# Kernel tuning notes

Measured on AMD Instinct MI355X. Metric: run time of the kernel, lower is better.

The kernel has to match this reference:

```python
import jax, jax.numpy as jnp
import numpy as np

N_NODES = 100000
IN_CH, HIDDEN, OUT_CH = 128, 128, 64
N_POS, N_NEG = 600000, 600000


def _glorot(key, shape):
    lim = float(np.sqrt(6.0 / (shape[0] + shape[1])))
    return jax.random.uniform(key, shape, jnp.float32, -lim, lim)


def setup_inputs() -> dict:
    key = jax.random.key(0)
    k = jax.random.split(key, 7)
    x = jax.random.normal(k[0], (N_NODES, IN_CH), jnp.float32)
    pos_edge_index = jax.random.randint(k[1], (2, N_POS), 0, N_NODES, jnp.int64)
    neg_edge_index = jax.random.randint(k[2], (2, N_NEG), 0, N_NODES, jnp.int64)
    W1 = _glorot(k[3], (IN_CH, HIDDEN))
    b1 = jnp.zeros((HIDDEN,), jnp.float32)
    W2 = _glorot(k[4], (HIDDEN, OUT_CH))
    b2 = jnp.zeros((OUT_CH,), jnp.float32)
    return {"x": x, "pos_edge_index": pos_edge_index, "neg_edge_index": neg_edge_index,
            "W1": W1, "b1": b1, "W2": W2, "b2": b2}


def gcn_conv(x, W, b, src, dst, n_nodes):
    # PyG GCNConv: add self-loops, symmetric deg^-1/2 normalization, linear, bias
    h = x @ W                                               # [N, F_out]
    ones = jnp.ones(src.shape, h.dtype)
    deg = jax.ops.segment_sum(ones, dst, num_segments=n_nodes) + 1.0  # self-loop
    dinv = jax.lax.rsqrt(deg)                               # deg^-0.5, deg >= 1
    norm = dinv[src] * dinv[dst]                            # per-edge norm
    agg = jax.ops.segment_sum(h[src] * norm[:, None], dst, num_segments=n_nodes)
    agg = agg + h * (dinv * dinv)[:, None]                  # self-loop messages
    return agg + b


def reference(x, pos_edge_index, neg_edge_index, W1, b1, W2, b2):
    n = x.shape[0]
    src, dst = pos_edge_index[0], pos_edge_index[1]
    z = gcn_conv(x, W1, b1, src, dst, n)
    z = jax.nn.relu(z)
    z = gcn_conv(z, W2, b2, src, dst, n)
    # decode: gather endpoints of pos+neg edges, elementwise product, sum over feat
    ei = jnp.concatenate([pos_edge_index, neg_edge_index], axis=-1)  # [2, E_pos+E_neg]
    return jnp.sum(z[ei[0]] * z[ei[1]], axis=-1)
```

## Files before the change

### kernel.cpp

```cpp
#include <hip/hip_runtime.h>

#define N_NODES 100000
#define IN_CH 128
#define HIDDEN 128
#define OUT_CH 64
#define N_POS 600000
#define N_NEG 600000

typedef unsigned int uint32;
typedef unsigned short ushort16;
typedef __attribute__((ext_vector_type(8))) short bf16x8;
typedef __attribute__((ext_vector_type(4))) float f32x4;

__device__ inline float bf_lo(uint32 u) {
    union { uint32 i; float f; } v;
    v.i = u << 16;
    return v.f;
}
__device__ inline float bf_hi(uint32 u) {
    union { uint32 i; float f; } v;
    v.i = u & 0xffff0000u;
    return v.f;
}
__device__ inline ushort16 f2bf(float f) {
    union { uint32 i; float f; } v;
    v.f = f;
    uint32 r = v.i + 0x7fffu + ((v.i >> 16) & 1u);
    return (ushort16)(r >> 16);
}
__device__ inline uint32 pack2bf(float a, float b) {
    return (uint32)f2bf(a) | ((uint32)f2bf(b) << 16);
}

__global__ void hist_count(const int* __restrict__ dst, int* __restrict__ hist, int n_edges) {
    int i = blockIdx.x * blockDim.x + threadIdx.x;
    if (i < n_edges) atomicAdd(&hist[dst[i]], 1);
}

__global__ void scan_reduce(const int* __restrict__ hist, int* __restrict__ partials, int n) {
    __shared__ int sdata[256];
    int b = blockIdx.x, t = threadIdx.x;
    int base = b * 1024;
    int s = 0;
    for (int i = t; i < 1024; i += 256) {
        int idx = base + i;
        s += (idx < n) ? hist[idx] : 0;
    }
    sdata[t] = s;
    __syncthreads();
    for (int off = 128; off > 0; off >>= 1) {
        if (t < off) sdata[t] += sdata[t + off];
        __syncthreads();
    }
    if (t == 0) partials[b] = sdata[0];
}

__global__ void scan_partials(int* __restrict__ partials, int nb) {
    __shared__ int tmp[128];
    int t = threadIdx.x;
    int v = (t < nb) ? partials[t] : 0;
    tmp[t] = v;
    __syncthreads();
    for (int off = 1; off < 128; off <<= 1) {
        int a = (t >= off) ? tmp[t - off] : 0;
        __syncthreads();
        tmp[t] += a;
        __syncthreads();
    }
    if (t < nb) partials[t] = tmp[t] - v;
}

__global__ void scan_final(const int* __restrict__ hist, const int* __restrict__ partials,
                           int* __restrict__ rowstart, int* __restrict__ cursor,
                           float* __restrict__ dinv, int n) {
    __shared__ int tsum[256];
    int t = threadIdx.x, b = blockIdx.x;
    int base = b * 1024 + t * 4;
    int v[4];
    int s = 0;
#pragma unroll
    for (int j = 0; j < 4; j++) {
        int i = base + j;
        v[j] = (i < n) ? hist[i] : 0;
        s += v[j];
    }
    tsum[t] = s;
    __syncthreads();
    for (int off = 1; off < 256; off <<= 1) {
        int a = (t >= off) ? tsum[t - off] : 0;
        __syncthreads();
        tsum[t] += a;
        __syncthreads();
    }
    int offset = partials[b] + (tsum[t] - s);
#pragma unroll
    for (int j = 0; j < 4; j++) {
        int i = base + j;
        if (i < n) {
            rowstart[i] = offset;
            cursor[i] = offset;
            dinv[i] = rsqrtf((float)v[j] + 1.0f);
            offset += v[j];
        }
    }
    if (b == 0 && t == 0) rowstart[n] = N_POS;
}

__global__ void csr_fill(const int* __restrict__ src, const int* __restrict__ dst,
                         const float* __restrict__ dinv, int* __restrict__ cursor,
                         int2* __restrict__ adjw, int n_edges) {
    int e = blockIdx.x * blockDim.x + threadIdx.x;
    if (e < n_edges) {
        int s = src[e], d = dst[e];
        int p = atomicAdd(&cursor[d], 1);
        adjw[p] = int2{s, __float_as_int(dinv[s] * dinv[d])};
    }
}

__global__ void wt_convert(const float* __restrict__ W1, const float* __restrict__ W2,
                           ushort16* __restrict__ W1t, ushort16* __restrict__ W2t) {
    int i = blockIdx.x * blockDim.x + threadIdx.x;
    if (i < 128 * 128) {
        int n = i >> 7, k = i & 127;
        W1t[i] = f2bf(W1[k * 128 + n]);
    } else {
        int j = i - 128 * 128;
        if (j < 64 * 128) {
            int n = j >> 7, k = j & 127;
            W2t[j] = f2bf(W2[k * 64 + n]);
        }
    }
}

template <int M, bool XBF>
__global__ __launch_bounds__(256) void gemm_mfma(const void* __restrict__ Xv,
                                                const ushort16* __restrict__ Wt,
                                                ushort16* __restrict__ H, int n) {
    constexpr int K = 128;
    constexpr int TN = 64;
    constexpr int XS = 136;
    __shared__ short Xs[TN * XS];
    __shared__ short Ws[M * XS];
    int tid = threadIdx.x;
    int node0 = blockIdx.x * TN;

    for (int q = tid; q < M * K / 8; q += 256) {
        int row = q >> 4;
        int c = q & 15;
        uint4 v = ((const uint4*)Wt)[q];
        *(uint4*)(Ws + row * XS + c * 8) = v;
    }
    if (!XBF) {
        const float* X = (const float*)Xv;
        int row = tid >> 2, part = tid & 3;
        int gn = node0 + row;
#pragma unroll
        for (int c = 0; c < 8; ++c) {
            int k = part * 32 + c * 4;
            float4 v = (gn < n) ? *(const float4*)(X + (size_t)gn * K + k) : float4{0, 0, 0, 0};
            uint2 p = {pack2bf(v.x, v.y), pack2bf(v.z, v.w)};
            *(uint2*)(Xs + row * XS + k) = p;
        }
    } else {
        const ushort16* X = (const ushort16*)Xv;
        for (int q = tid; q < TN * K / 8; q += 256) {
            int row = q >> 4;
            int c = q & 15;
            int gn = node0 + row;
            uint4 v = (gn < n) ? ((const uint4*)(X + (size_t)gn * K))[c] : uint4{0, 0, 0, 0};
            *(uint4*)(Xs + row * XS + c * 8) = v;
        }
    }
    __syncthreads();

    constexpr int CT = M / 16;
    int w = tid >> 6;
    int lane = tid & 63;
    int l15 = lane & 15;
    int quad = lane >> 4;

    f32x4 acc[CT] = {};
    const short* xrow = Xs + (w * 16 + l15) * XS + quad * 8;
#pragma unroll
    for (int kk = 0; kk < 4; ++kk) {
        bf16x8 a = *(const bf16x8*)(xrow + kk * 32);
#pragma unroll
        for (int ct = 0; ct < CT; ++ct) {
            bf16x8 b = *(const bf16x8*)(Ws + (ct * 16 + l15) * XS + quad * 8 + kk * 32);
            acc[ct] = __builtin_amdgcn_mfma_f32_16x16x32_bf16(a, b, acc[ct], 0, 0, 0);
        }
    }

#pragma unroll
    for (int ct = 0; ct < CT; ++ct) {
#pragma unroll
        for (int r = 0; r < 4; ++r) {
            int gn = node0 + w * 16 + quad * 4 + r;
            if (gn < n) H[(size_t)gn * M + ct * 16 + l15] = f2bf(acc[ct][r]);
        }
    }
}

template <int F, bool RELU>
__global__ void agg_pull(const int* __restrict__ rowstart, const int2* __restrict__ adjw,
                         const float* __restrict__ dinv, const ushort16* __restrict__ H,
                         const float* __restrict__ bias, ushort16* __restrict__ Z, int n) {
    int g = threadIdx.x >> 4;
    int l = threadIdx.x & 15;
    int node = blockIdx.x * (blockDim.x >> 4) + g;
    if (node >= n) return;
    float dn = dinv[node];
    int rs = rowstart[node], re = rowstart[node + 1];
    if (F == 128) {
        float ac[4][8] = {};
        int p = rs;
        for (; p + 4 <= re; p += 4) {
            int2 e0 = adjw[p], e1 = adjw[p + 1], e2 = adjw[p + 2], e3 = adjw[p + 3];
            uint4 h0 = *(const uint4*)(H + (size_t)e0.x * F + l * 8);
            uint4 h1 = *(const uint4*)(H + (size_t)e1.x * F + l * 8);
            uint4 h2 = *(const uint4*)(H + (size_t)e2.x * F + l * 8);
            uint4 h3 = *(const uint4*)(H + (size_t)e3.x * F + l * 8);
            float w0 = __int_as_float(e0.y), w1 = __int_as_float(e1.y);
            float w2 = __int_as_float(e2.y), w3 = __int_as_float(e3.y);
            ac[0][0] += bf_lo(h0.x) * w0; ac[0][1] += bf_hi(h0.x) * w0;
            ac[0][2] += bf_lo(h0.y) * w0; ac[0][3] += bf_hi(h0.y) * w0;
            ac[0][4] += bf_lo(h0.z) * w0; ac[0][5] += bf_hi(h0.z) * w0;
            ac[0][6] += bf_lo(h0.w) * w0; ac[0][7] += bf_hi(h0.w) * w0;
            ac[1][0] += bf_lo(h1.x) * w1; ac[1][1] += bf_hi(h1.x) * w1;
            ac[1][2] += bf_lo(h1.y) * w1; ac[1][3] += bf_hi(h1.y) * w1;
            ac[1][4] += bf_lo(h1.z) * w1; ac[1][5] += bf_hi(h1.z) * w1;
            ac[1][6] += bf_lo(h1.w) * w1; ac[1][7] += bf_hi(h1.w) * w1;
            ac[2][0] += bf_lo(h2.x) * w2; ac[2][1] += bf_hi(h2.x) * w2;
            ac[2][2] += bf_lo(h2.y) * w2; ac[2][3] += bf_hi(h2.y) * w2;
            ac[2][4] += bf_lo(h2.z) * w2; ac[2][5] += bf_hi(h2.z) * w2;
            ac[2][6] += bf_lo(h2.w) * w2; ac[2][7] += bf_hi(h2.w) * w2;
            ac[3][0] += bf_lo(h3.x) * w3; ac[3][1] += bf_hi(h3.x) * w3;
            ac[3][2] += bf_lo(h3.y) * w3; ac[3][3] += bf_hi(h3.y) * w3;
            ac[3][4] += bf_lo(h3.z) * w3; ac[3][5] += bf_hi(h3.z) * w3;
            ac[3][6] += bf_lo(h3.w) * w3; ac[3][7] += bf_hi(h3.w) * w3;
        }
        for (; p < re; ++p) {
            int2 e = adjw[p];
            float w = __int_as_float(e.y);
            uint4 h = *(const uint4*)(H + (size_t)e.x * F + l * 8);
            ac[0][0] += bf_lo(h.x) * w; ac[0][1] += bf_hi(h.x) * w;
            ac[0][2] += bf_lo(h.y) * w; ac[0][3] += bf_hi(h.y) * w;
            ac[0][4] += bf_lo(h.z) * w; ac[0][5] += bf_hi(h.z) * w;
            ac[0][6] += bf_lo(h.w) * w; ac[0][7] += bf_hi(h.w) * w;
        }
        uint4 hv = *(const uint4*)(H + (size_t)node * F + l * 8);
        float4 bv0 = *(const float4*)(bias + l * 8);
        float4 bv1 = *(const float4*)(bias + l * 8 + 4);
        float d2 = dn * dn;
        float v[8];
        float hs[8] = {bf_lo(hv.x), bf_hi(hv.x), bf_lo(hv.y), bf_hi(hv.y),
                       bf_lo(hv.z), bf_hi(hv.z), bf_lo(hv.w), bf_hi(hv.w)};
        float bb[8] = {bv0.x, bv0.y, bv0.z, bv0.w, bv1.x, bv1.y, bv1.z, bv1.w};
#pragma unroll
        for (int j = 0; j < 8; ++j) {
            v[j] = (ac[0][j] + ac[1][j]) + (ac[2][j] + ac[3][j]) + hs[j] * d2 + bb[j];
            if (RELU) v[j] = fmaxf(v[j], 0.0f);
        }
        *(uint4*)(Z + (size_t)node * F + l * 8) =
            uint4{pack2bf(v[0], v[1]), pack2bf(v[2], v[3]), pack2bf(v[4], v[5]),
                  pack2bf(v[6], v[7])};
    } else {
        float ac[4][4] = {};
        int p = rs;
        for (; p + 4 <= re; p += 4) {
            int2 e0 = adjw[p], e1 = adjw[p + 1], e2 = adjw[p + 2], e3 = adjw[p + 3];
            uint2 h0 = *(const uint2*)(H + (size_t)e0.x * F + l * 4);
            uint2 h1 = *(const uint2*)(H + (size_t)e1.x * F + l * 4);
            uint2 h2 = *(const uint2*)(H + (size_t)e2.x * F + l * 4);
            uint2 h3 = *(const uint2*)(H + (size_t)e3.x * F + l * 4);
            float w0 = __int_as_float(e0.y), w1 = __int_as_float(e1.y);
            float w2 = __int_as_float(e2.y), w3 = __int_as_float(e3.y);
            ac[0][0] += bf_lo(h0.x) * w0; ac[0][1] += bf_hi(h0.x) * w0;
            ac[0][2] += bf_lo(h0.y) * w0; ac[0][3] += bf_hi(h0.y) * w0;
            ac[1][0] += bf_lo(h1.x) * w1; ac[1][1] += bf_hi(h1.x) * w1;
            ac[1][2] += bf_lo(h1.y) * w1; ac[1][3] += bf_hi(h1.y) * w1;
            ac[2][0] += bf_lo(h2.x) * w2; ac[2][1] += bf_hi(h2.x) * w2;
            ac[2][2] += bf_lo(h2.y) * w2; ac[2][3] += bf_hi(h2.y) * w2;
            ac[3][0] += bf_lo(h3.x) * w3; ac[3][1] += bf_hi(h3.x) * w3;
            ac[3][2] += bf_lo(h3.y) * w3; ac[3][3] += bf_hi(h3.y) * w3;
        }
        for (; p < re; ++p) {
            int2 e = adjw[p];
            float w = __int_as_float(e.y);
            uint2 h = *(const uint2*)(H + (size_t)e.x * F + l * 4);
            ac[0][0] += bf_lo(h.x) * w; ac[0][1] += bf_hi(h.x) * w;
            ac[0][2] += bf_lo(h.y) * w; ac[0][3] += bf_hi(h.y) * w;
        }
        uint2 hv = *(const uint2*)(H + (size_t)node * F + l * 4);
        float4 bv = *(const float4*)(bias + l * 4);
        float d2 = dn * dn;
        float hs[4] = {bf_lo(hv.x), bf_hi(hv.x), bf_lo(hv.y), bf_hi(hv.y)};
        float bb[4] = {bv.x, bv.y, bv.z, bv.w};
        float v[4];
#pragma unroll
        for (int j = 0; j < 4; ++j) {
            v[j] = (ac[0][j] + ac[1][j]) + (ac[2][j] + ac[3][j]) + hs[j] * d2 + bb[j];
            if (RELU) v[j] = fmaxf(v[j], 0.0f);
        }
        *(uint2*)(Z + (size_t)node * F + l * 4) = uint2{pack2bf(v[0], v[1]), pack2bf(v[2], v[3])};
    }
}

__global__ void decode_mfma(const int* __restrict__ pos, const int* __restrict__ neg,
                            const short* __restrict__ Z, float* __restrict__ out) {
    int wid = threadIdx.x >> 6;
    int lane = threadIdx.x & 63;
    int l15 = lane & 15;
    int quad = lane >> 4;
    int e0 = (blockIdx.x * 4 + wid) * 16;
    if (e0 >= N_POS + N_NEG) return;
    const int* bp = (e0 < N_POS) ? pos : (neg - N_POS);
    int e = e0 + l15;
    int a = bp[e];
    int b = bp[600000 + e];

    const short* za = Z + (size_t)a * OUT_CH + quad * 8;
    const short* zb = Z + (size_t)b * OUT_CH + quad * 8;
    bf16x8 a0 = *(const bf16x8*)(za);
    bf16x8 a1 = *(const bf16x8*)(za + 32);
    bf16x8 b0 = *(const bf16x8*)(zb);
    bf16x8 b1 = *(const bf16x8*)(zb + 32);

    f32x4 acc = {};
    acc = __builtin_amdgcn_mfma_f32_16x16x32_bf16(a0, b0, acc, 0, 0, 0);
    acc = __builtin_amdgcn_mfma_f32_16x16x32_bf16(a1, b1, acc, 0, 0, 0);

    if (quad == (l15 >> 2)) out[e] = acc[l15 & 3];
}

extern "C" void kernel_launch(void* const* d_in, const int* in_sizes, int n_in,
                              void* d_out, int out_size, void* d_ws, size_t ws_size,
                              hipStream_t stream) {
    const float* x = (const float*)d_in[0];
    const int* pos = (const int*)d_in[1];
    const int* neg = (const int*)d_in[2];
    const float* W1 = (const float*)d_in[3];
    const float* b1 = (const float*)d_in[4];
    const float* W2 = (const float*)d_in[5];
    const float* b2 = (const float*)d_in[6];
    float* out = (float*)d_out;

    ushort16* A = (ushort16*)d_ws;
    ushort16* B = A + (size_t)N_NODES * 128;
    float* dinv = (float*)(B + (size_t)N_NODES * 128);
    int* hist = (int*)(dinv + N_NODES);
    int* rowstart = hist + N_NODES;
    int* cursor = rowstart + N_NODES + 1;
    int2* adjw = (int2*)(cursor + N_NODES);
    int* partials = (int*)(adjw + N_POS);
    ushort16* W1t = (ushort16*)(partials + 128);
    ushort16* W2t = W1t + 128 * 128;

    const int* pos_src = pos;
    const int* pos_dst = pos + N_POS;

    constexpr int NB_SCAN = (N_NODES + 1023) / 1024;

    hipMemsetAsync(hist, 0, N_NODES * sizeof(int), stream);
    hist_count<<<(N_POS + 255) / 256, 256, 0, stream>>>(pos_dst, hist, N_POS);
    scan_reduce<<<NB_SCAN, 256, 0, stream>>>(hist, partials, N_NODES);
    scan_partials<<<1, 128, 0, stream>>>(partials, NB_SCAN);
    scan_final<<<NB_SCAN, 256, 0, stream>>>(hist, partials, rowstart, cursor, dinv, N_NODES);
    csr_fill<<<(N_POS + 255) / 256, 256, 0, stream>>>(pos_src, pos_dst, dinv, cursor, adjw,
                                                      N_POS);
    wt_convert<<<(128 * 128 + 64 * 128 + 255) / 256, 256, 0, stream>>>(W1, W2, W1t, W2t);

    gemm_mfma<HIDDEN, false><<<(N_NODES + 63) / 64, 256, 0, stream>>>(x, W1t, A, N_NODES);
    agg_pull<HIDDEN, true><<<(N_NODES + 15) / 16, 256, 0, stream>>>(rowstart, adjw, dinv, A, b1,
                                                                    B, N_NODES);

    ushort16* h2 = A;
    gemm_mfma<OUT_CH, true><<<(N_NODES + 63) / 64, 256, 0, stream>>>(B, W2t, h2, N_NODES);
    ushort16* z2 = B;
    agg_pull<OUT_CH, false><<<(N_NODES + 15) / 16, 256, 0, stream>>>(rowstart, adjw, dinv, h2, b2,
                                                                     z2, N_NODES);

    decode_mfma<<<(N_POS + N_NEG) / 64, 256, 0, stream>>>(pos, neg, (const short*)z2, out);
}
```

Baseline: 289.6 us.

## Fold scan partials into scan_final, merge fill kernels, predicate aggregation, widen decode

Removes the separate partial-scan launch by having each scan_final block sum the preceding partials with a wave reduction. It also merges csr_fill and the weight conversion into one launch. The aggregation kernels now issue the first 8 neighbour gathers unconditionally, using clamped indices and zero weights, to get more loads in flight for low-degree nodes. The decode kernel handles 32 edges per wave with interleaved MFMAs. Together these cut launch count and raise memory-level parallelism, at the cost of redundant loads for nodes with fewer than 8 neighbours.

```diff
diff --git a/kernel.cpp b/kernel.cpp
--- a/kernel.cpp
+++ b/kernel.cpp
@@ -55,26 +55,21 @@
     if (t == 0) partials[b] = sdata[0];
 }
 
-__global__ void scan_partials(int* __restrict__ partials, int nb) {
-    __shared__ int tmp[128];
-    int t = threadIdx.x;
-    int v = (t < nb) ? partials[t] : 0;
-    tmp[t] = v;
-    __syncthreads();
-    for (int off = 1; off < 128; off <<= 1) {
-        int a = (t >= off) ? tmp[t - off] : 0;
-        __syncthreads();
-        tmp[t] += a;
-        __syncthreads();
-    }
-    if (t < nb) partials[t] = tmp[t] - v;
-}
-
 __global__ void scan_final(const int* __restrict__ hist, const int* __restrict__ partials,
                            int* __restrict__ rowstart, int* __restrict__ cursor,
                            float* __restrict__ dinv, int n) {
     __shared__ int tsum[256];
+    __shared__ int base_sh;
     int t = threadIdx.x, b = blockIdx.x;
+    if (t < 64) {
+        int s0 = (t < b) ? partials[t] : 0;
+        int i2 = t + 64;
+        int s1 = (i2 < b && i2 < 98) ? partials[i2] : 0;
+        int s = s0 + s1;
+#pragma unroll
+        for (int off = 32; off > 0; off >>= 1) s += __shfl_down(s, off, 64);
+        if (t == 0) base_sh = s;
+    }
     int base = b * 1024 + t * 4;
     int v[4];
     int s = 0;
@@ -92,7 +87,7 @@
         tsum[t] += a;
         __syncthreads();
     }
-    int offset = partials[b] + (tsum[t] - s);
+    int offset = base_sh + (tsum[t] - s);
 #pragma unroll
     for (int j = 0; j < 4; j++) {
         int i = base + j;
@@ -106,28 +101,30 @@
     if (b == 0 && t == 0) rowstart[n] = N_POS;
 }
 
-__global__ void csr_fill(const int* __restrict__ src, const int* __restrict__ dst,
-                         const float* __restrict__ dinv, int* __restrict__ cursor,
-                         int2* __restrict__ adjw, int n_edges) {
-    int e = blockIdx.x * blockDim.x + threadIdx.x;
-    if (e < n_edges) {
-        int s = src[e], d = dst[e];
-        int p = atomicAdd(&cursor[d], 1);
-        adjw[p] = int2{s, __float_as_int(dinv[s] * dinv[d])};
-    }
-}
-
-__global__ void wt_convert(const float* __restrict__ W1, const float* __restrict__ W2,
-                           ushort16* __restrict__ W1t, ushort16* __restrict__ W2t) {
-    int i = blockIdx.x * blockDim.x + threadIdx.x;
-    if (i < 128 * 128) {
-        int n = i >> 7, k = i & 127;
-        W1t[i] = f2bf(W1[k * 128 + n]);
+#define NB_FILL ((N_POS + 255) / 256)
+__global__ void csr_fill_wt(const int* __restrict__ src, const int* __restrict__ dst,
+                            const float* __restrict__ dinv, int* __restrict__ cursor,
+                            int2* __restrict__ adjw, const float* __restrict__ W1,
+                            const float* __restrict__ W2, ushort16* __restrict__ W1t,
+                            ushort16* __restrict__ W2t) {
+    if (blockIdx.x < NB_FILL) {
+        int e = blockIdx.x * 256 + threadIdx.x;
+        if (e < N_POS) {
+            int s = src[e], d = dst[e];
+            int p = atomicAdd(&cursor[d], 1);
+            adjw[p] = int2{s, __float_as_int(dinv[s] * dinv[d])};
+        }
     } else {
-        int j = i - 128 * 128;
-        if (j < 64 * 128) {
-            int n = j >> 7, k = j & 127;
-            W2t[j] = f2bf(W2[k * 64 + n]);
+        int i = (blockIdx.x - NB_FILL) * 256 + threadIdx.x;
+        if (i < 128 * 128) {
+            int n = i >> 7, k = i & 127;
+            W1t[i] = f2bf(W1[k * 128 + n]);
+        } else {
+            int j = i - 128 * 128;
+            if (j < 64 * 128) {
+                int n = j >> 7, k = j & 127;
+                W2t[j] = f2bf(W2[k * 64 + n]);
+            }
         }
     }
 }
@@ -211,85 +208,79 @@
     if (node >= n) return;
     float dn = dinv[node];
     int rs = rowstart[node], re = rowstart[node + 1];
+    int deg = re - rs;
+    int pc = (deg > 0) ? rs : (rs > 0 ? rs - 1 : 0);
     if (F == 128) {
-        float ac[4][8] = {};
-        int p = rs;
-        for (; p + 4 <= re; p += 4) {
-            int2 e0 = adjw[p], e1 = adjw[p + 1], e2 = adjw[p + 2], e3 = adjw[p + 3];
-            uint4 h0 = *(const uint4*)(H + (size_t)e0.x * F + l * 8);
-            uint4 h1 = *(const uint4*)(H + (size_t)e1.x * F + l * 8);
-            uint4 h2 = *(const uint4*)(H + (size_t)e2.x * F + l * 8);
-            uint4 h3 = *(const uint4*)(H + (size_t)e3.x * F + l * 8);
-            float w0 = __int_as_float(e0.y), w1 = __int_as_float(e1.y);
-            float w2 = __int_as_float(e2.y), w3 = __int_as_float(e3.y);
-            ac[0][0] += bf_lo(h0.x) * w0; ac[0][1] += bf_hi(h0.x) * w0;
-            ac[0][2] += bf_lo(h0.y) * w0; ac[0][3] += bf_hi(h0.y) * w0;
-            ac[0][4] += bf_lo(h0.z) * w0; ac[0][5] += bf_hi(h0.z) * w0;
-            ac[0][6] += bf_lo(h0.w) * w0; ac[0][7] += bf_hi(h0.w) * w0;
-            ac[1][0] += bf_lo(h1.x) * w1; ac[1][1] += bf_hi(h1.x) * w1;
-            ac[1][2] += bf_lo(h1.y) * w1; ac[1][3] += bf_hi(h1.y) * w1;
-            ac[1][4] += bf_lo(h1.z) * w1; ac[1][5] += bf_hi(h1.z) * w1;
-            ac[1][6] += bf_lo(h1.w) * w1; ac[1][7] += bf_hi(h1.w) * w1;
-            ac[2][0] += bf_lo(h2.x) * w2; ac[2][1] += bf_hi(h2.x) * w2;
-            ac[2][2] += bf_lo(h2.y) * w2; ac[2][3] += bf_hi(h2.y) * w2;
-            ac[2][4] += bf_lo(h2.z) * w2; ac[2][5] += bf_hi(h2.z) * w2;
-            ac[2][6] += bf_lo(h2.w) * w2; ac[2][7] += bf_hi(h2.w) * w2;
-            ac[3][0] += bf_lo(h3.x) * w3; ac[3][1] += bf_hi(h3.x) * w3;
-            ac[3][2] += bf_lo(h3.y) * w3; ac[3][3] += bf_hi(h3.y) * w3;
-            ac[3][4] += bf_lo(h3.z) * w3; ac[3][5] += bf_hi(h3.z) * w3;
-            ac[3][6] += bf_lo(h3.w) * w3; ac[3][7] += bf_hi(h3.w) * w3;
-        }
-        for (; p < re; ++p) {
+        uint4 h[8];
+        float wv[8];
+#pragma unroll
+        for (int j = 0; j < 8; ++j) {
+            int p = (rs + j < re) ? rs + j : pc;
+            int2 e = adjw[p];
+            h[j] = *(const uint4*)(H + (size_t)e.x * F + l * 8);
+            wv[j] = (j < deg) ? __int_as_float(e.y) : 0.0f;
+        }
+        float s0[8] = {}, s1[8] = {};
+#pragma unroll
+        for (int j = 0; j < 8; j += 2) {
+            s0[0] += bf_lo(h[j].x) * wv[j]; s0[1] += bf_hi(h[j].x) * wv[j];
+            s0[2] += bf_lo(h[j].y) * wv[j]; s0[3] += bf_hi(h[j].y) * wv[j];
+            s0[4] += bf_lo(h[j].z) * wv[j]; s0[5] += bf_hi(h[j].z) * wv[j];
+            s0[6] += bf_lo(h[j].w) * wv[j]; s0[7] += bf_hi(h[j].w) * wv[j];
+            s1[0] += bf_lo(h[j + 1].x) * wv[j + 1]; s1[1] += bf_hi(h[j + 1].x) * wv[j + 1];
+            s1[2] += bf_lo(h[j + 1].y) * wv[j + 1]; s1[3] += bf_hi(h[j + 1].y) * wv[j + 1];
+            s1[4] += bf_lo(h[j + 1].z) * wv[j + 1]; s1[5] += bf_hi(h[j + 1].z) * wv[j + 1];
+            s1[6] += bf_lo(h[j + 1].w) * wv[j + 1]; s1[7] += bf_hi(h[j + 1].w) * wv[j + 1];
+        }
+        for (int p = rs + 8; p < re; ++p) {
             int2 e = adjw[p];
             float w = __int_as_float(e.y);
-            uint4 h = *(const uint4*)(H + (size_t)e.x * F + l * 8);
-            ac[0][0] += bf_lo(h.x) * w; ac[0][1] += bf_hi(h.x) * w;
-            ac[0][2] += bf_lo(h.y) * w; ac[0][3] += bf_hi(h.y) * w;
-            ac[0][4] += bf_lo(h.z) * w; ac[0][5] += bf_hi(h.z) * w;
-            ac[0][6] += bf_lo(h.w) * w; ac[0][7] += bf_hi(h.w) * w;
+            uint4 hh = *(const uint4*)(H + (size_t)e.x * F + l * 8);
+            s0[0] += bf_lo(hh.x) * w; s0[1] += bf_hi(hh.x) * w;
+            s0[2] += bf_lo(hh.y) * w; s0[3] += bf_hi(hh.y) * w;
+            s0[4] += bf_lo(hh.z) * w; s0[5] += bf_hi(hh.z) * w;
+            s0[6] += bf_lo(hh.w) * w; s0[7] += bf_hi(hh.w) * w;
         }
         uint4 hv = *(const uint4*)(H + (size_t)node * F + l * 8);
         float4 bv0 = *(const float4*)(bias + l * 8);
         float4 bv1 = *(const float4*)(bias + l * 8 + 4);
         float d2 = dn * dn;
-        float v[8];
         float hs[8] = {bf_lo(hv.x), bf_hi(hv.x), bf_lo(hv.y), bf_hi(hv.y),
                        bf_lo(hv.z), bf_hi(hv.z), bf_lo(hv.w), bf_hi(hv.w)};
         float bb[8] = {bv0.x, bv0.y, bv0.z, bv0.w, bv1.x, bv1.y, bv1.z, bv1.w};
+        float v[8];
 #pragma unroll
         for (int j = 0; j < 8; ++j) {
-            v[j] = (ac[0][j] + ac[1][j]) + (ac[2][j] + ac[3][j]) + hs[j] * d2 + bb[j];
+            v[j] = s0[j] + s1[j] + hs[j] * d2 + bb[j];
             if (RELU) v[j] = fmaxf(v[j], 0.0f);
         }
         *(uint4*)(Z + (size_t)node * F + l * 8) =
             uint4{pack2bf(v[0], v[1]), pack2bf(v[2], v[3]), pack2bf(v[4], v[5]),
                   pack2bf(v[6], v[7])};
     } else {
-        float ac[4][4] = {};
-        int p = rs;
-        for (; p + 4 <= re; p += 4) {
-            int2 e0 = adjw[p], e1 = adjw[p + 1], e2 = adjw[p + 2], e3 = adjw[p + 3];
-            uint2 h0 = *(const uint2*)(H + (size_t)e0.x * F + l * 4);
-            uint2 h1 = *(const uint2*)(H + (size_t)e1.x * F + l * 4);
-            uint2 h2 = *(const uint2*)(H + (size_t)e2.x * F + l * 4);
-            uint2 h3 = *(const uint2*)(H + (size_t)e3.x * F + l * 4);
-            float w0 = __int_as_float(e0.y), w1 = __int_as_float(e1.y);
-            float w2 = __int_as_float(e2.y), w3 = __int_as_float(e3.y);
-            ac[0][0] += bf_lo(h0.x) * w0; ac[0][1] += bf_hi(h0.x) * w0;
-            ac[0][2] += bf_lo(h0.y) * w0; ac[0][3] += bf_hi(h0.y) * w0;
-            ac[1][0] += bf_lo(h1.x) * w1; ac[1][1] += bf_hi(h1.x) * w1;
-            ac[1][2] += bf_lo(h1.y) * w1; ac[1][3] += bf_hi(h1.y) * w1;
-            ac[2][0] += bf_lo(h2.x) * w2; ac[2][1] += bf_hi(h2.x) * w2;
-            ac[2][2] += bf_lo(h2.y) * w2; ac[2][3] += bf_hi(h2.y) * w2;
-            ac[3][0] += bf_lo(h3.x) * w3; ac[3][1] += bf_hi(h3.x) * w3;
-            ac[3][2] += bf_lo(h3.y) * w3; ac[3][3] += bf_hi(h3.y) * w3;
-        }
-        for (; p < re; ++p) {
+        uint2 h[8];
+        float wv[8];
+#pragma unroll
+        for (int j = 0; j < 8; ++j) {
+            int p = (rs + j < re) ? rs + j : pc;
+            int2 e = adjw[p];
+            h[j] = *(const uint2*)(H + (size_t)e.x * F + l * 4);
+            wv[j] = (j < deg) ? __int_as_float(e.y) : 0.0f;
+        }
+        float s0[4] = {}, s1[4] = {};
+#pragma unroll
+        for (int j = 0; j < 8; j += 2) {
+            s0[0] += bf_lo(h[j].x) * wv[j]; s0[1] += bf_hi(h[j].x) * wv[j];
+            s0[2] += bf_lo(h[j].y) * wv[j]; s0[3] += bf_hi(h[j].y) * wv[j];
+            s1[0] += bf_lo(h[j + 1].x) * wv[j + 1]; s1[1] += bf_hi(h[j + 1].x) * wv[j + 1];
+            s1[2] += bf_lo(h[j + 1].y) * wv[j + 1]; s1[3] += bf_hi(h[j + 1].y) * wv[j + 1];
+        }
+        for (int p = rs + 8; p < re; ++p) {
             int2 e = adjw[p];
             float w = __int_as_float(e.y);
-            uint2 h = *(const uint2*)(H + (size_t)e.x * F + l * 4);
-            ac[0][0] += bf_lo(h.x) * w; ac[0][1] += bf_hi(h.x) * w;
-            ac[0][2] += bf_lo(h.y) * w; ac[0][3] += bf_hi(h.y) * w;
+            uint2 hh = *(const uint2*)(H + (size_t)e.x * F + l * 4);
+            s0[0] += bf_lo(hh.x) * w; s0[1] += bf_hi(hh.x) * w;
+            s0[2] += bf_lo(hh.y) * w; s0[3] += bf_hi(hh.y) * w;
         }
         uint2 hv = *(const uint2*)(H + (size_t)node * F + l * 4);
         float4 bv = *(const float4*)(bias + l * 4);
@@ -299,7 +290,7 @@
         float v[4];
 #pragma unroll
         for (int j = 0; j < 4; ++j) {
-            v[j] = (ac[0][j] + ac[1][j]) + (ac[2][j] + ac[3][j]) + hs[j] * d2 + bb[j];
+            v[j] = s0[j] + s1[j] + hs[j] * d2 + bb[j];
             if (RELU) v[j] = fmaxf(v[j], 0.0f);
         }
         *(uint2*)(Z + (size_t)node * F + l * 4) = uint2{pack2bf(v[0], v[1]), pack2bf(v[2], v[3])};
@@ -312,25 +303,37 @@
     int lane = threadIdx.x & 63;
     int l15 = lane & 15;
     int quad = lane >> 4;
-    int e0 = (blockIdx.x * 4 + wid) * 16;
+    int e0 = (blockIdx.x * 4 + wid) * 32;
     if (e0 >= N_POS + N_NEG) return;
     const int* bp = (e0 < N_POS) ? pos : (neg - N_POS);
-    int e = e0 + l15;
-    int a = bp[e];
-    int b = bp[600000 + e];
-
-    const short* za = Z + (size_t)a * OUT_CH + quad * 8;
-    const short* zb = Z + (size_t)b * OUT_CH + quad * 8;
-    bf16x8 a0 = *(const bf16x8*)(za);
-    bf16x8 a1 = *(const bf16x8*)(za + 32);
-    bf16x8 b0 = *(const bf16x8*)(zb);
-    bf16x8 b1 = *(const bf16x8*)(zb + 32);
-
-    f32x4 acc = {};
-    acc = __builtin_amdgcn_mfma_f32_16x16x32_bf16(a0, b0, acc, 0, 0, 0);
-    acc = __builtin_amdgcn_mfma_f32_16x16x32_bf16(a1, b1, acc, 0, 0, 0);
-
-    if (quad == (l15 >> 2)) out[e] = acc[l15 & 3];
+    int eA = e0 + l15;
+    int eB = e0 + 16 + l15;
+    int aA = bp[eA], bA = bp[600000 + eA];
+    int aB = bp[eB], bB = bp[600000 + eB];
+
+    const short* zaA = Z + (size_t)aA * OUT_CH + quad * 8;
+    const short* zbA = Z + (size_t)bA * OUT_CH + quad * 8;
+    const short* zaB = Z + (size_t)aB * OUT_CH + quad * 8;
+    const short* zbB = Z + (size_t)bB * OUT_CH + quad * 8;
+    bf16x8 a0A = *(const bf16x8*)(zaA);
+    bf16x8 a1A = *(const bf16x8*)(zaA + 32);
+    bf16x8 b0A = *(const bf16x8*)(zbA);
+    bf16x8 b1A = *(const bf16x8*)(zbA + 32);
+    bf16x8 a0B = *(const bf16x8*)(zaB);
+    bf16x8 a1B = *(const bf16x8*)(zaB + 32);
+    bf16x8 b0B = *(const bf16x8*)(zbB);
+    bf16x8 b1B = *(const bf16x8*)(zbB + 32);
+
+    f32x4 accA = {}, accB = {};
+    accA = __builtin_amdgcn_mfma_f32_16x16x32_bf16(a0A, b0A, accA, 0, 0, 0);
+    accB = __builtin_amdgcn_mfma_f32_16x16x32_bf16(a0B, b0B, accB, 0, 0, 0);
+    accA = __builtin_amdgcn_mfma_f32_16x16x32_bf16(a1A, b1A, accA, 0, 0, 0);
+    accB = __builtin_amdgcn_mfma_f32_16x16x32_bf16(a1B, b1B, accB, 0, 0, 0);
+
+    if (quad == (l15 >> 2)) {
+        out[eA] = accA[l15 & 3];
+        out[eB] = accB[l15 & 3];
+    }
 }
 
 extern "C" void kernel_launch(void* const* d_in, const int* in_sizes, int n_in,
@@ -364,11 +367,9 @@
     hipMemsetAsync(hist, 0, N_NODES * sizeof(int), stream);
     hist_count<<<(N_POS + 255) / 256, 256, 0, stream>>>(pos_dst, hist, N_POS);
     scan_reduce<<<NB_SCAN, 256, 0, stream>>>(hist, partials, N_NODES);
-    scan_partials<<<1, 128, 0, stream>>>(partials, NB_SCAN);
     scan_final<<<NB_SCAN, 256, 0, stream>>>(hist, partials, rowstart, cursor, dinv, N_NODES);
-    csr_fill<<<(N_POS + 255) / 256, 256, 0, stream>>>(pos_src, pos_dst, dinv, cursor, adjw,
-                                                      N_POS);
-    wt_convert<<<(128 * 128 + 64 * 128 + 255) / 256, 256, 0, stream>>>(W1, W2, W1t, W2t);
+    csr_fill_wt<<<NB_FILL + 96, 256, 0, stream>>>(pos_src, pos_dst, dinv, cursor, adjw, W1, W2,
+                                                  W1t, W2t);
 
     gemm_mfma<HIDDEN, false><<<(N_NODES + 63) / 64, 256, 0, stream>>>(x, W1t, A, N_NODES);
     agg_pull<HIDDEN, true><<<(N_NODES + 15) / 16, 256, 0, stream>>>(rowstart, adjw, dinv, A, b1,
@@ -380,5 +381,5 @@
     agg_pull<OUT_CH, false><<<(N_NODES + 15) / 16, 256, 0, stream>>>(rowstart, adjw, dinv, h2, b2,
                                                                      z2, N_NODES);
 
-    decode_mfma<<<(N_POS + N_NEG) / 64, 256, 0, stream>>>(pos, neg, (const short*)z2, out);
-}
+    decode_mfma<<<(N_POS + N_NEG) / 128, 256, 0, stream>>>(pos, neg, (const short*)z2, out);
+}
```

Result: no change. 285.0 us (-1.6%).
